# Kernel tuning notes

Hardware: AMD Instinct MI355X
Metric: run time of the kernel (lower is better)

Reference implementation:

```python
import jax, jax.numpy as jnp
import numpy as np

N = 1024                      # FFT length (init kwarg)
NF = N // 2 + 1               # rfft output length = len(freq)
PB_LO = 40.0 / 60.0           # pulse_band[0] in Hz
PB_HI = 180.0 / 60.0          # pulse_band[1] in Hz
DELTA_HZ = 6.0 / 60.0         # self.delta after /60
W0, W1 = 1.0, 1.0             # weights[0], weights[1]
B, T = 32768, 1024


def setup_inputs() -> dict:
    key = jax.random.key(0)
    k1, k2 = jax.random.split(key)
    preds = jax.random.normal(k1, (B, T), dtype=jnp.float32)
    # realistic camera frame rates ~25-35 Hz (must exceed 2*pulse_band[1]=6 Hz)
    Fs = 25.0 + 10.0 * jax.random.uniform(k2, (B,), dtype=jnp.float32)
    return {"preds": preds, "Fs": Fs}


def reference(preds, Fs):
    idx = jnp.arange(NF)                                            # [Nf]
    # freq = linspace(0, Fs/2, Nf) per sample -> [B, Nf]
    freq = (Fs[:, None] * 0.5) * (idx.astype(jnp.float32) / (NF - 1))
    left = jnp.argmin(jnp.abs(freq - PB_LO), axis=1)                # [B] int
    right = jnp.argmin(jnp.abs(freq - PB_HI), axis=1)               # [B] int

    psd = jnp.abs(jnp.fft.rfft(preds, n=N)) ** 2                    # [B, Nf]
    total = jnp.sum(psd, axis=-1)                                   # [B]

    l = left[:, None]
    r = right[:, None]
    out_band = (idx < l) | (idx >= r)                               # psd[:left] + psd[right:]
    band_loss = jnp.sum(jnp.where(out_band, psd, 0.0), axis=-1) / (1e-8 + total)

    in_band = (idx >= l) & (idx < r)
    # argmax(psd[left:right]) + left  (psd >= 0, so -inf mask is safe)
    peak = jnp.argmax(jnp.where(in_band, psd, -jnp.inf), axis=1)    # [B]
    # delta = max(1, round(self.delta / (Fs/2/len(freq))))  (round half-to-even, as Python)
    delta = jnp.maximum(1.0, jnp.round(DELTA_HZ / (Fs * 0.5 / NF))).astype(jnp.int32)

    p = peak[:, None]
    d = delta[:, None]
    # psd[left:peak-delta] + psd[peak+delta:right]  (empty slices -> 0 via mask)
    sparse_mask = in_band & ((idx < p - d) | (idx >= p + d))
    num = jnp.sum(jnp.where(sparse_mask, psd, 0.0), axis=-1)
    # sum(psd[left:right] + 1e-8) adds 1e-8 per in-band bin, keep faithful
    den = jnp.sum(jnp.where(in_band, psd + 1e-8, 0.0), axis=-1)
    sparse_loss = num / den

    return W0 * jnp.mean(band_loss) + W1 * jnp.mean(sparse_loss)
```

## Files before the change

kernel.cpp:

```cpp
#include <hip/hip_runtime.h>
#include <cmath>

#define BATCH 32768

struct cplx { float x, y; };
__device__ __forceinline__ cplx cadd(cplx a, cplx b){ return {a.x+b.x, a.y+b.y}; }
__device__ __forceinline__ cplx csub(cplx a, cplx b){ return {a.x-b.x, a.y-b.y}; }
__device__ __forceinline__ cplx cmul(cplx a, cplx b){ return {a.x*b.x - a.y*b.y, a.x*b.y + a.y*b.x}; }
__device__ __forceinline__ cplx cmul_mi(cplx a){ return {a.y, -a.x}; }
__device__ __forceinline__ cplx cmul_w81(cplx a){ const float c=0.70710678f; return {c*(a.x+a.y), c*(a.y-a.x)}; }
__device__ __forceinline__ cplx cmul_w83(cplx a){ const float c=0.70710678f; return {c*(a.y-a.x), -c*(a.x+a.y)}; }

__device__ __forceinline__ void dft8(cplx a[8]) {
    cplx t0=cadd(a[0],a[4]), t4=csub(a[0],a[4]);
    cplx t1=cadd(a[1],a[5]), t5=csub(a[1],a[5]);
    cplx t2=cadd(a[2],a[6]), t6=csub(a[2],a[6]);
    cplx t3=cadd(a[3],a[7]), t7=csub(a[3],a[7]);
    cplx u0=cadd(t0,t2), u2=csub(t0,t2);
    cplx u1=cadd(t1,t3), u3=cmul_mi(csub(t1,t3));
    a[0]=cadd(u0,u1); a[4]=csub(u0,u1); a[2]=cadd(u2,u3); a[6]=csub(u2,u3);
    cplx v0=t4, v1=cmul_w81(t5), v2=cmul_mi(t6), v3=cmul_w83(t7);
    cplx w0=cadd(v0,v2), w2=csub(v0,v2);
    cplx w1=cadd(v1,v3), w3=cmul_mi(csub(v1,v3));
    a[1]=cadd(w0,w1); a[5]=csub(w0,w1); a[3]=cadd(w2,w3); a[7]=csub(w2,w3);
}

__device__ __forceinline__ int nearest_bin(float fs, float target) {
    float x = target * 1024.0f / fs;
    int i0 = (int)floorf(x);
    int lo = max(0, i0 - 1), hi = min(512, i0 + 2);
    int bi = lo; float bd = 1e30f;
    for (int i = lo; i <= hi; ++i) {
        float fr = (fs * 0.5f) * ((float)i / 512.0f);
        float d = fabsf(fr - target);
        if (d < bd) { bd = d; bi = i; }
    }
    return bi;
}

__global__ __launch_bounds__(256) void fft_loss_kernel(
    const float* __restrict__ preds, const float* __restrict__ Fs,
    float* __restrict__ blockpartial)
{
    __shared__ float sre[4][576];
    __shared__ float sim[4][576];
    __shared__ float sblk[4];

    const int tid  = threadIdx.x;
    const int wv   = tid >> 6;
    const int lane = tid & 63;
    const int row  = blockIdx.x * 4 + wv;

    float* re = sre[wv];
    float* im = sim[wv];

    const float2* x2 = reinterpret_cast<const float2*>(preds) + (size_t)row * 512;

    cplx z[8];
#pragma unroll
    for (int n1 = 0; n1 < 8; ++n1) {
        float2 v = x2[n1 * 64 + lane];
        z[n1] = {v.x, v.y};
    }
    dft8(z);
    {
        float sb, cb;
        __sincosf(-0.012271846f * (float)lane, &sb, &cb);
        cplx w = {cb, sb}, u = w;
#pragma unroll
        for (int r = 1; r < 8; ++r) { z[r] = cmul(z[r], u); u = cmul(u, w); }
    }
#pragma unroll
    for (int r = 0; r < 8; ++r) { re[r*72 + lane] = z[r].x; im[r*72 + lane] = z[r].y; }

    const int rB = lane & 7, m0 = lane >> 3;
    cplx b[8];
#pragma unroll
    for (int m1 = 0; m1 < 8; ++m1) {
        int a = rB*72 + 8*m1 + m0;
        b[m1] = {re[a], im[a]};
    }
    dft8(b);
    {
        float sb, cb;
        __sincosf(-0.09817477f * (float)m0, &sb, &cb);
        cplx w = {cb, sb}, u = w;
#pragma unroll
        for (int s = 1; s < 8; ++s) { b[s] = cmul(b[s], u); u = cmul(u, w); }
    }
#pragma unroll
    for (int s = 0; s < 8; ++s) {
        int a = rB*72 + 8*m0 + ((s + m0) & 7);
        re[a] = b[s].x; im[a] = b[s].y;
    }

    const int sC = lane >> 3;
    cplx c[8];
#pragma unroll
    for (int m = 0; m < 8; ++m) {
        int a = rB*72 + 8*m + ((sC + m) & 7);
        c[m] = {re[a], im[a]};
    }
    dft8(c);
#pragma unroll
    for (int t = 0; t < 8; ++t) { re[lane + 64*t] = c[t].x; im[lane + 64*t] = c[t].y; }

    const float fs  = Fs[row];
    const int left  = nearest_bin(fs, (float)(40.0/60.0));
    const int right = nearest_bin(fs, 3.0f);

    float psd[8];
    float total = 0.f, inb = 0.f, best = -1.f;
    int besti = 1 << 30;
    float sk, ck;
    __sincosf(-0.0061359233f * (float)lane, &sk, &ck);
    cplx wk = {ck, sk};
    const cplx wstep = {0.92387953f, -0.38268343f};
#pragma unroll
    for (int t = 0; t < 8; ++t) {
        int k  = lane + 64*t;
        cplx a  = {re[k], im[k]};
        int k2 = (512 - k) & 511;
        cplx bb = {re[k2], -im[k2]};
        float ex = 0.5f*(a.x + bb.x), ey = 0.5f*(a.y + bb.y);
        float dx = a.x - bb.x,        dy = a.y - bb.y;
        float ox = 0.5f*dy,           oy = -0.5f*dx;
        float Xr = ex + wk.x*ox - wk.y*oy;
        float Xi = ey + wk.x*oy + wk.y*ox;
        float v  = Xr*Xr + Xi*Xi;
        psd[t] = v;
        total += v;
        if (k >= left && k < right) {
            inb += v;
            if (v > best) { best = v; besti = k; }
        }
        wk = cmul(wk, wstep);
    }
    float psd512 = 0.f;
    if (lane == 0) {
        float d = re[0] - im[0];
        psd512 = d*d;
        total += psd512;
    }
#pragma unroll
    for (int t = 0; t < 8; ++t) im[lane + 64*t] = psd[t];
    if (lane == 0) im[512] = psd512;

#pragma unroll
    for (int off = 32; off > 0; off >>= 1) {
        total += __shfl_down(total, off);
        inb   += __shfl_down(inb, off);
        float ob = __shfl_down(best, off);
        int   oi = __shfl_down(besti, off);
        if (ob > best || (ob == best && oi < besti)) { best = ob; besti = oi; }
    }
    if (lane == 0) {
        int delta = (int)rintf(0.1f / ((fs * 0.5f) / 513.0f));
        if (delta < 1) delta = 1;
        int lo = max(left, besti - delta), hi = min(right, besti + delta);
        float wsum = 0.f;
        for (int f = lo; f < hi; ++f) wsum += im[f];
        float band = (total - inb) / (1e-8f + total);
        float den  = inb + 1e-8f * (float)(right - left);
        sblk[wv] = band + (inb - wsum) / den;
    }
    __syncthreads();
    if (tid == 0) blockpartial[blockIdx.x] = sblk[0] + sblk[1] + sblk[2] + sblk[3];
}

__global__ __launch_bounds__(1024) void reduce_kernel(
    const float* __restrict__ bp, float* __restrict__ out)
{
    __shared__ float w[16];
    const int t = threadIdx.x;
    float acc = 0.f;
#pragma unroll
    for (int i = 0; i < 8; ++i) acc += bp[t + 1024*i];
    for (int off = 32; off > 0; off >>= 1) acc += __shfl_down(acc, off);
    const int lane = t & 63, wvi = t >> 6;
    if (lane == 0) w[wvi] = acc;
    __syncthreads();
    if (t == 0) {
        float s = 0.f;
        for (int i = 0; i < 16; ++i) s += w[i];
        out[0] = s * (1.0f / (float)BATCH);
    }
}

extern "C" void kernel_launch(void* const* d_in, const int* in_sizes, int n_in,
                              void* d_out, int out_size, void* d_ws, size_t ws_size,
                              hipStream_t stream) {
    const float* preds = (const float*)d_in[0];
    const float* Fs    = (const float*)d_in[1];
    float* bp          = (float*)d_ws;
    float* out         = (float*)d_out;

    fft_loss_kernel<<<BATCH / 4, 256, 0, stream>>>(preds, Fs, bp);
    reduce_kernel<<<1, 1024, 0, stream>>>(bp, out);
}
```

Baseline: 191.3 us.

## Pack LDS as float2, pair mirror bins via shuffles, parallelize window sum

Shared memory moves from separate real/imag arrays to interleaved float2 with a padded row stride. The last FFT stage no longer writes its output back to LDS. The mirrored bin k2=512-k needed for the real-FFT post-processing is taken from register values via wave shuffles, with lane 0 handling its own wraparound case. The peak-window sum is computed in parallel across lanes from registers and reduced with shuffles, replacing lane 0's serial loop over LDS. This removes LDS round trips and a serial tail, at the cost of extra shuffle instructions.

```diff
diff --git a/kernel.cpp b/kernel.cpp
--- a/kernel.cpp
+++ b/kernel.cpp
@@ -2,6 +2,7 @@
 #include <cmath>
 
 #define BATCH 32768
+#define SROW 66
 
 struct cplx { float x, y; };
 __device__ __forceinline__ cplx cadd(cplx a, cplx b){ return {a.x+b.x, a.y+b.y}; }
@@ -42,8 +43,7 @@
     const float* __restrict__ preds, const float* __restrict__ Fs,
     float* __restrict__ blockpartial)
 {
-    __shared__ float sre[4][576];
-    __shared__ float sim[4][576];
+    __shared__ float2 lds[4][8 * SROW];
     __shared__ float sblk[4];
 
     const int tid  = threadIdx.x;
@@ -51,9 +51,7 @@
     const int lane = tid & 63;
     const int row  = blockIdx.x * 4 + wv;
 
-    float* re = sre[wv];
-    float* im = sim[wv];
-
+    float2* sm = lds[wv];
     const float2* x2 = reinterpret_cast<const float2*>(preds) + (size_t)row * 512;
 
     cplx z[8];
@@ -71,14 +69,14 @@
         for (int r = 1; r < 8; ++r) { z[r] = cmul(z[r], u); u = cmul(u, w); }
     }
 #pragma unroll
-    for (int r = 0; r < 8; ++r) { re[r*72 + lane] = z[r].x; im[r*72 + lane] = z[r].y; }
+    for (int r = 0; r < 8; ++r) sm[r * SROW + lane] = make_float2(z[r].x, z[r].y);
 
     const int rB = lane & 7, m0 = lane >> 3;
     cplx b[8];
 #pragma unroll
     for (int m1 = 0; m1 < 8; ++m1) {
-        int a = rB*72 + 8*m1 + m0;
-        b[m1] = {re[a], im[a]};
+        float2 v = sm[rB * SROW + 8 * m1 + m0];
+        b[m1] = {v.x, v.y};
     }
     dft8(b);
     {
@@ -90,24 +88,22 @@
     }
 #pragma unroll
     for (int s = 0; s < 8; ++s) {
-        int a = rB*72 + 8*m0 + ((s + m0) & 7);
-        re[a] = b[s].x; im[a] = b[s].y;
+        sm[rB * SROW + 8 * m0 + ((s + m0) & 7)] = make_float2(b[s].x, b[s].y);
     }
 
     const int sC = lane >> 3;
     cplx c[8];
 #pragma unroll
     for (int m = 0; m < 8; ++m) {
-        int a = rB*72 + 8*m + ((sC + m) & 7);
-        c[m] = {re[a], im[a]};
+        float2 v = sm[rB * SROW + 8 * m + ((sC + m) & 7)];
+        c[m] = {v.x, v.y};
     }
     dft8(c);
-#pragma unroll
-    for (int t = 0; t < 8; ++t) { re[lane + 64*t] = c[t].x; im[lane + 64*t] = c[t].y; }
 
     const float fs  = Fs[row];
-    const int left  = nearest_bin(fs, (float)(40.0/60.0));
+    const int left  = nearest_bin(fs, (float)(40.0 / 60.0));
     const int right = nearest_bin(fs, 3.0f);
+    const int pl    = (64 - lane) & 63;
 
     float psd[8];
     float total = 0.f, inb = 0.f, best = -1.f;
@@ -118,33 +114,29 @@
     const cplx wstep = {0.92387953f, -0.38268343f};
 #pragma unroll
     for (int t = 0; t < 8; ++t) {
-        int k  = lane + 64*t;
-        cplx a  = {re[k], im[k]};
-        int k2 = (512 - k) & 511;
-        cplx bb = {re[k2], -im[k2]};
-        float ex = 0.5f*(a.x + bb.x), ey = 0.5f*(a.y + bb.y);
-        float dx = a.x - bb.x,        dy = a.y - bb.y;
-        float ox = 0.5f*dy,           oy = -0.5f*dx;
-        float Xr = ex + wk.x*ox - wk.y*oy;
-        float Xi = ey + wk.x*oy + wk.y*ox;
-        float v  = Xr*Xr + Xi*Xi;
+        cplx a = c[t];
+        float px = __shfl(c[7 - t].x, pl);
+        float py = __shfl(c[7 - t].y, pl);
+        if (lane == 0) { px = c[(8 - t) & 7].x; py = c[(8 - t) & 7].y; }
+        float ex = 0.5f * (a.x + px), ey = 0.5f * (a.y - py);
+        float dx = a.x - px,          dy = a.y + py;
+        float ox = 0.5f * dy,         oy = -0.5f * dx;
+        float Xr = ex + wk.x * ox - wk.y * oy;
+        float Xi = ey + wk.x * oy + wk.y * ox;
+        float v  = Xr * Xr + Xi * Xi;
         psd[t] = v;
         total += v;
+        int k = lane + 64 * t;
         if (k >= left && k < right) {
             inb += v;
             if (v > best) { best = v; besti = k; }
         }
         wk = cmul(wk, wstep);
     }
-    float psd512 = 0.f;
     if (lane == 0) {
-        float d = re[0] - im[0];
-        psd512 = d*d;
-        total += psd512;
-    }
-#pragma unroll
-    for (int t = 0; t < 8; ++t) im[lane + 64*t] = psd[t];
-    if (lane == 0) im[512] = psd512;
+        float d = c[0].x - c[0].y;
+        total += d * d;
+    }
 
 #pragma unroll
     for (int off = 32; off > 0; off >>= 1) {
@@ -154,12 +146,20 @@
         int   oi = __shfl_down(besti, off);
         if (ob > best || (ob == best && oi < besti)) { best = ob; besti = oi; }
     }
+    const int bbi = __shfl(besti, 0);
+    int delta = (int)rintf(0.1f / ((fs * 0.5f) / 513.0f));
+    if (delta < 1) delta = 1;
+    const int lo = max(left, bbi - delta), hi = min(right, bbi + delta);
+    float wsum = 0.f;
+#pragma unroll
+    for (int t = 0; t < 8; ++t) {
+        int k = lane + 64 * t;
+        if (k >= lo && k < hi) wsum += psd[t];
+    }
+#pragma unroll
+    for (int off = 32; off > 0; off >>= 1) wsum += __shfl_down(wsum, off);
+
     if (lane == 0) {
-        int delta = (int)rintf(0.1f / ((fs * 0.5f) / 513.0f));
-        if (delta < 1) delta = 1;
-        int lo = max(left, besti - delta), hi = min(right, besti + delta);
-        float wsum = 0.f;
-        for (int f = lo; f < hi; ++f) wsum += im[f];
         float band = (total - inb) / (1e-8f + total);
         float den  = inb + 1e-8f * (float)(right - left);
         sblk[wv] = band + (inb - wsum) / den;
@@ -175,7 +175,7 @@
     const int t = threadIdx.x;
     float acc = 0.f;
 #pragma unroll
-    for (int i = 0; i < 8; ++i) acc += bp[t + 1024*i];
+    for (int i = 0; i < 8; ++i) acc += bp[t + 1024 * i];
     for (int off = 32; off > 0; off >>= 1) acc += __shfl_down(acc, off);
     const int lane = t & 63, wvi = t >> 6;
     if (lane == 0) w[wvi] = acc;
```

New measurement: 194.5 us. About the same (+1.7%).
